# Kernel tuning notes

Hardware: AMD Instinct MI355X
Metric: run time of the kernel (lower is better)

## Reference

```python
import jax, jax.numpy as jnp
import numpy as np
from jax import lax

TOPK = 80
RADIUS_GAIN = 14.0
RADIUS_MIN = 1.5
RADIUS_MAX = 18.0


def _norm01(x, eps=1e-6):
    b = x.shape[0]
    flat = x.reshape(b, -1)
    mn = flat.min(axis=1).reshape(b, 1, 1, 1)
    mx = flat.max(axis=1).reshape(b, 1, 1, 1)
    return (x - mn) / (mx - mn + eps)


def _avg_pool9(x):
    # kernel 9, stride 1, pad 4, count_include_pad=True (torch default)
    s = lax.reduce_window(x, 0.0, lax.add, (1, 1, 9, 9), (1, 1, 1, 1),
                          [(0, 0), (0, 0), (4, 4), (4, 4)])
    return s / 81.0


def _max_pool5(x):
    return lax.reduce_window(x, -jnp.inf, lax.max, (1, 1, 5, 5), (1, 1, 1, 1),
                             [(0, 0), (0, 0), (2, 2), (2, 2)])


def setup_inputs() -> dict:
    key = jax.random.key(0)
    k1, k2 = jax.random.split(key)
    B, H, W = 8, 256, 256
    voxel_score_map = jax.random.uniform(k1, (B, 1, H, W), dtype=jnp.float32)
    depth = jax.random.uniform(k2, (B, 1, H, W), dtype=jnp.float32)
    return {"voxel_score_map": voxel_score_map, "depth": depth}


def reference(voxel_score_map, depth):
    dtype = voxel_score_map.dtype
    b, _, h, w = voxel_score_map.shape

    # _compact_connected_prior
    occ = (voxel_score_map > 0.2).astype(dtype)
    local_occ = _avg_pool9(occ)
    local_mass = _avg_pool9(voxel_score_map)
    compact = _norm01(local_occ * local_mass)
    score_map = voxel_score_map * compact

    # _gaussian_map: 5x5 max-pool NMS -> per-image top-k peaks
    pooled = _max_pool5(score_map)
    maxima = score_map * (score_map == pooled).astype(dtype)
    flat = maxima[:, 0].reshape(b, h * w)          # [b, h*w]
    vals, inds = lax.top_k(flat, TOPK)             # [b, k]
    vals = jnp.where(vals > 0, vals, jnp.zeros_like(vals))  # masked peaks splat 0
    ys = (inds // w).astype(dtype)
    xs = (inds % w).astype(dtype)

    z = jnp.take_along_axis(depth[:, 0].reshape(b, h * w), inds, axis=1)
    z = jnp.maximum(z, 0.001)
    radius = jnp.clip(RADIUS_GAIN / z, RADIUS_MIN, RADIUS_MAX)  # [b, k]
    sigma2 = (0.6 * radius) ** 2                                 # [b, k]

    yy = jnp.arange(h, dtype=dtype)
    xx = jnp.arange(w, dtype=dtype)
    dx = xx[None, None, None, :] - xs[:, :, None, None]   # [b, k, 1, w]
    dy = yy[None, None, :, None] - ys[:, :, None, None]   # [b, k, h, 1]
    d2 = dx ** 2 + dy ** 2                                 # [b, k, h, w]
    maps = vals[:, :, None, None] * jnp.exp(-d2 / (2.0 * sigma2[:, :, None, None] + 1e-6))
    gauss = maps.max(axis=1)[:, None]                      # [b, 1, h, w]
    return _norm01(gauss)
```

## Files before the change

kernel.cpp:

```cpp
#include <hip/hip_runtime.h>
#include <float.h>
#include <math.h>

#define BB 8
#define HH 256
#define WW 256
#define NPIX 65536
#define TOT (BB*NPIX)
#define KTOP 80
#define NTIL 64
#define TCAP 128
#define CAP 8192
#define SELBINS 4096
#define BNDCAP 4096
#define NBLK (BB*NTIL)
typedef unsigned long long ull;

__global__ void k_box9(const float* __restrict__ vsm, float* __restrict__ prod,
                       float* __restrict__ pmn, float* __restrict__ pmx,
                       unsigned* __restrict__ histg, unsigned* __restrict__ bcnt) {
    int blk = blockIdx.x;
    int b = blk >> 6, t = blk & 63;
    int ty0 = (t >> 3) << 5, tx0 = (t & 7) << 5;
    int tid = threadIdx.x;

    if (tid < 64) histg[b * SELBINS + t * 64 + tid] = 0u;
    if (blk < BB && tid == 0) bcnt[blk] = 0u;

    __shared__ float val[40][40];
    __shared__ float rs_o[40][32];
    __shared__ float rs_m[40][32];
    for (int i = tid; i < 1600; i += 256) {
        int ly = i / 40, lx = i - ly * 40;
        int gy = ty0 - 4 + ly, gx = tx0 - 4 + lx;
        float v = 0.f;
        if (gy >= 0 && gy < HH && gx >= 0 && gx < WW) v = vsm[(b * HH + gy) * WW + gx];
        val[ly][lx] = v;
    }
    __syncthreads();
    for (int i = tid; i < 1280; i += 256) {
        int ly = i >> 5, lx = i & 31;
        float so = 0.f, sm = 0.f;
        #pragma unroll
        for (int d = 0; d < 9; ++d) { float v = val[ly][lx + d]; so += (v > 0.2f) ? 1.f : 0.f; sm += v; }
        rs_o[ly][lx] = so; rs_m[ly][lx] = sm;
    }
    __syncthreads();
    int ox = tid & 31, oy0 = (tid >> 5) << 2;
    float tmn = FLT_MAX, tmx = -FLT_MAX;
    #pragma unroll
    for (int j = 0; j < 4; ++j) {
        int oy = oy0 + j;
        float so = 0.f, sm = 0.f;
        #pragma unroll
        for (int d = 0; d < 9; ++d) { so += rs_o[oy + d][ox]; sm += rs_m[oy + d][ox]; }
        float p = (so * (1.f / 81.f)) * (sm * (1.f / 81.f));
        prod[(b * HH + ty0 + oy) * WW + tx0 + ox] = p;
        tmn = fminf(tmn, p); tmx = fmaxf(tmx, p);
    }
    __shared__ float smn[256], smx[256];
    smn[tid] = tmn; smx[tid] = tmx;
    __syncthreads();
    for (int off = 128; off > 0; off >>= 1) {
        if (tid < off) { smn[tid] = fminf(smn[tid], smn[tid + off]); smx[tid] = fmaxf(smx[tid], smx[tid + off]); }
        __syncthreads();
    }
    if (tid == 0) { pmn[blk] = smn[0]; pmx[blk] = smx[0]; }
}

__global__ void k_nms(const float* __restrict__ vsm, const float* __restrict__ prod,
                      const float* __restrict__ pmn, const float* __restrict__ pmx,
                      unsigned* __restrict__ bcnt, float* __restrict__ candV,
                      int* __restrict__ candI, unsigned* __restrict__ histg) {
    int blk = blockIdx.x;
    int b = blk >> 6, t = blk & 63;
    int ty0 = (t >> 3) << 5, tx0 = (t & 7) << 5;
    int tid = threadIdx.x;
    __shared__ float sred[2];
    if (tid < 64) {
        float mn = pmn[b * NTIL + tid];
        float mx = pmx[b * NTIL + tid];
        #pragma unroll
        for (int o = 32; o > 0; o >>= 1) { mn = fminf(mn, __shfl_xor(mn, o, 64)); mx = fmaxf(mx, __shfl_xor(mx, o, 64)); }
        if (tid == 0) { sred[0] = mn; sred[1] = mx; }
    }
    __syncthreads();
    float mnp = sred[0];
    float inv = 1.f / (sred[1] - mnp + 1e-6f);
    __shared__ float sc[36][36];
    __shared__ float hm[36][32];
    for (int i = tid; i < 1296; i += 256) {
        int ly = i / 36, lx = i - ly * 36;
        int gy = ty0 - 2 + ly, gx = tx0 - 2 + lx;
        float s = -FLT_MAX;
        if (gy >= 0 && gy < HH && gx >= 0 && gx < WW) {
            int idx = (b * HH + gy) * WW + gx;
            s = vsm[idx] * ((prod[idx] - mnp) * inv);
        }
        sc[ly][lx] = s;
    }
    __syncthreads();
    for (int i = tid; i < 1152; i += 256) {
        int ly = i >> 5, lx = i & 31;
        float m = sc[ly][lx];
        #pragma unroll
        for (int d = 1; d < 5; ++d) m = fmaxf(m, sc[ly][lx + d]);
        hm[ly][lx] = m;
    }
    __syncthreads();
    __shared__ unsigned scnt;
    __shared__ unsigned sbase;
    __shared__ float bv[TCAP];
    __shared__ int bi[TCAP];
    if (tid == 0) scnt = 0;
    __syncthreads();
    int ox = tid & 31, oy0 = (tid >> 5) << 2;
    #pragma unroll
    for (int j = 0; j < 4; ++j) {
        int oy = oy0 + j;
        float m = hm[oy][ox];
        #pragma unroll
        for (int d = 1; d < 5; ++d) m = fmaxf(m, hm[oy + d][ox]);
        float s = sc[oy + 2][ox + 2];
        if (s == m && s > 0.f) {
            unsigned p = atomicAdd(&scnt, 1u);
            if (p < TCAP) { bv[p] = s; bi[p] = (ty0 + oy) * WW + tx0 + ox; }
        }
    }
    __syncthreads();
    unsigned cnt = min(scnt, (unsigned)TCAP);
    if (tid == 0) sbase = cnt ? atomicAdd(&bcnt[b], cnt) : 0u;
    __syncthreads();
    unsigned base = sbase;
    for (unsigned i = tid; i < cnt; i += 256) {
        unsigned pos = base + i;
        if (pos < CAP) {
            float v = bv[i];
            candV[b * CAP + pos] = v;
            candI[b * CAP + pos] = bi[i];
            atomicAdd(&histg[b * SELBINS + (__float_as_uint(v) >> 19)], 1u);
        }
    }
}

__global__ void __launch_bounds__(1024)
k_topk(const float* __restrict__ depth, const unsigned* __restrict__ bcnt,
       const float* __restrict__ candV, const int* __restrict__ candI,
       const unsigned* __restrict__ histg, float4* __restrict__ pk) {
    int b = blockIdx.x;
    int tid = threadIdx.x;
    __shared__ unsigned sc[1024];
    __shared__ ull bnd[BNDCAP];
    __shared__ ull acc[KTOP];
    __shared__ int sBin;
    __shared__ unsigned nAccS, nBndS;

    const unsigned* hg = histg + b * SELBINS;
    int j0 = tid * 4;
    unsigned h0 = hg[j0], h1 = hg[j0 + 1], h2 = hg[j0 + 2], h3 = hg[j0 + 3];
    unsigned part = h0 + h1 + h2 + h3;
    sc[tid] = part;
    if (tid == 0) { sBin = 0; nAccS = 0; nBndS = 0; }
    __syncthreads();
    for (int off = 1; off < 1024; off <<= 1) {
        unsigned v = (tid + off < 1024) ? sc[tid + off] : 0u;
        __syncthreads();
        sc[tid] += v;
        __syncthreads();
    }
    unsigned excl = sc[tid] - part;
    unsigned suf3 = excl + h3, suf2 = suf3 + h2, suf1 = suf2 + h1, suf0 = suf1 + h0;
    if (suf0 >= KTOP && suf0 - h0 < KTOP) sBin = j0;
    if (suf1 >= KTOP && suf1 - h1 < KTOP) sBin = j0 + 1;
    if (suf2 >= KTOP && suf2 - h2 < KTOP) sBin = j0 + 2;
    if (suf3 >= KTOP && suf3 - h3 < KTOP) sBin = j0 + 3;
    __syncthreads();
    int B = sBin;

    int nC = min((int)bcnt[b], CAP);
    for (int i = tid; i < nC; i += 1024) {
        float v = candV[b * CAP + i];
        unsigned bits = __float_as_uint(v);
        int bin = (int)(bits >> 19);
        if (bin >= B) {
            ull key = ((ull)bits << 32) | (ull)(0xFFFFFFFFu - (unsigned)candI[b * CAP + i]);
            if (bin > B) {
                unsigned p = atomicAdd(&nAccS, 1u);
                if (p < KTOP) acc[p] = key;
            } else {
                unsigned q = atomicAdd(&nBndS, 1u);
                if (q < BNDCAP) bnd[q] = key;
            }
        }
    }
    __syncthreads();
    unsigned nAcc = min(nAccS, (unsigned)KTOP);
    unsigned nBnd = min(nBndS, (unsigned)BNDCAP);
    unsigned quota = (KTOP > nAcc) ? (KTOP - nAcc) : 0u;
    if (quota > nBnd) quota = nBnd;

    for (int i = tid; i < (int)nBnd; i += 1024) {
        ull mykey = bnd[i];
        unsigned rank = 0;
        for (unsigned j = 0; j < nBnd; ++j) rank += (bnd[j] > mykey) ? 1u : 0u;
        if (rank < quota) acc[nAcc + rank] = mykey;
    }
    __syncthreads();

    if (tid < KTOP) {
        unsigned nTot = nAcc + quota;
        ull key = ((unsigned)tid < nTot) ? acc[tid] : 0ull;
        float plog = -INFINITY, fx = 0.f, fy = 0.f, c = 0.f;
        if (key) {
            unsigned bits = (unsigned)(key >> 32);
            int idx = (int)(0xFFFFFFFFu - (unsigned)(key & 0xFFFFFFFFu));
            float val = __uint_as_float(bits);
            plog = log2f(val);
            fx = (float)(idx & 255);
            fy = (float)(idx >> 8);
            float z = fmaxf(depth[b * NPIX + idx], 0.001f);
            float r = fminf(fmaxf(14.f / z, 1.5f), 18.f);
            float s2 = 0.36f * r * r;
            c = 1.44269504f / (2.f * s2 + 1e-6f);
        }
        pk[b * KTOP + tid] = make_float4(plog, fx, fy, c);
    }
}

__global__ void k_splat(const float4* __restrict__ pk, float* __restrict__ gauss,
                        float* __restrict__ gmn, float* __restrict__ gmx) {
    int blk = blockIdx.x;
    int b = blk >> 6;
    int y0 = (blk & 63) << 2;
    int x = threadIdx.x;
    __shared__ float4 lp[KTOP];
    if (x < KTOP) lp[x] = pk[b * KTOP + x];
    __syncthreads();
    float fx = (float)x, fy = (float)y0;
    float g0 = -INFINITY, g1 = -INFINITY, g2 = -INFINITY, g3 = -INFINITY;
    #pragma unroll 4
    for (int k = 0; k < KTOP; ++k) {
        float4 q = lp[k];
        float dx = fx - q.y;
        float dx2 = dx * dx;
        float dy = fy - q.z;
        float d2;
        d2 = fmaf(dy, dy, dx2);        g0 = fmaxf(g0, fmaf(-d2, q.w, q.x));
        float dyb = dy + 1.f;
        d2 = fmaf(dyb, dyb, dx2);      g1 = fmaxf(g1, fmaf(-d2, q.w, q.x));
        float dyc = dy + 2.f;
        d2 = fmaf(dyc, dyc, dx2);      g2 = fmaxf(g2, fmaf(-d2, q.w, q.x));
        float dyd = dy + 3.f;
        d2 = fmaf(dyd, dyd, dx2);      g3 = fmaxf(g3, fmaf(-d2, q.w, q.x));
    }
    float v0 = exp2f(g0), v1 = exp2f(g1), v2 = exp2f(g2), v3 = exp2f(g3);
    int base = (b * HH + y0) * WW + x;
    gauss[base] = v0; gauss[base + WW] = v1; gauss[base + 2 * WW] = v2; gauss[base + 3 * WW] = v3;
    float tmn = fminf(fminf(v0, v1), fminf(v2, v3));
    float tmx = fmaxf(fmaxf(v0, v1), fmaxf(v2, v3));
    __shared__ float smn[256], smx[256];
    smn[x] = tmn; smx[x] = tmx;
    __syncthreads();
    for (int off = 128; off > 0; off >>= 1) {
        if (x < off) { smn[x] = fminf(smn[x], smn[x + off]); smx[x] = fmaxf(smx[x], smx[x + off]); }
        __syncthreads();
    }
    if (x == 0) { gmn[blk] = smn[0]; gmx[blk] = smx[0]; }
}

__global__ void k_norm(const float* __restrict__ gauss, const float* __restrict__ gmn,
                       const float* __restrict__ gmx, float* __restrict__ out) {
    int blk = blockIdx.x;
    int b = blk >> 6;
    int tid = threadIdx.x;
    __shared__ float sred[2];
    if (tid < 64) {
        float mn = gmn[b * NTIL + tid];
        float mx = gmx[b * NTIL + tid];
        #pragma unroll
        for (int o = 32; o > 0; o >>= 1) { mn = fminf(mn, __shfl_xor(mn, o, 64)); mx = fmaxf(mx, __shfl_xor(mx, o, 64)); }
        if (tid == 0) { sred[0] = mn; sred[1] = mx; }
    }
    __syncthreads();
    float mn = sred[0];
    float inv = 1.f / (sred[1] - mn + 1e-6f);
    int i = blk * 256 + tid;
    float4 v = ((const float4*)gauss)[i];
    v.x = (v.x - mn) * inv;
    v.y = (v.y - mn) * inv;
    v.z = (v.z - mn) * inv;
    v.w = (v.w - mn) * inv;
    ((float4*)out)[i] = v;
}

extern "C" void kernel_launch(void* const* d_in, const int* in_sizes, int n_in,
                              void* d_out, int out_size, void* d_ws, size_t ws_size,
                              hipStream_t stream) {
    const float* vsm   = (const float*)d_in[0];
    const float* depth = (const float*)d_in[1];
    float* out = (float*)d_out;

    float4* pk   = (float4*)d_ws;
    float* prod  = (float*)(pk + BB * KTOP);
    float* gauss = prod + TOT;
    float* pmn   = gauss + TOT;
    float* pmx   = pmn + NBLK;
    float* gmn   = pmx + NBLK;
    float* gmx   = gmn + NBLK;
    unsigned* bcnt  = (unsigned*)(gmx + NBLK);
    unsigned* histg = bcnt + BB;
    float* candV = (float*)(histg + BB * SELBINS);
    int*   candI = (int*)(candV + BB * CAP);

    k_box9 <<<NBLK, 256, 0, stream>>>(vsm, prod, pmn, pmx, histg, bcnt);
    k_nms  <<<NBLK, 256, 0, stream>>>(vsm, prod, pmn, pmx, bcnt, candV, candI, histg);
    k_topk <<<BB, 1024, 0, stream>>>(depth, bcnt, candV, candI, histg, pk);
    k_splat<<<NBLK, 256, 0, stream>>>(pk, gauss, gmn, gmx);
    k_norm <<<NBLK, 256, 0, stream>>>(gauss, gmn, gmx, out);
}
```

Measured before the change: 42.96 us.

## Fold normalisation into splat using peak max and cull far peaks per row band

```diff
diff --git a/kernel.cpp b/kernel.cpp
--- a/kernel.cpp
+++ b/kernel.cpp
@@ -17,7 +17,7 @@
 typedef unsigned long long ull;
 
 __global__ void k_box9(const float* __restrict__ vsm, float* __restrict__ prod,
-                       float* __restrict__ pmn, float* __restrict__ pmx,
+                       float* __restrict__ pmn,
                        unsigned* __restrict__ histg, unsigned* __restrict__ bcnt) {
     int blk = blockIdx.x;
     int b = blk >> 6, t = blk & 63;
@@ -47,7 +47,7 @@
     }
     __syncthreads();
     int ox = tid & 31, oy0 = (tid >> 5) << 2;
-    float tmn = FLT_MAX, tmx = -FLT_MAX;
+    float tmn = FLT_MAX;
     #pragma unroll
     for (int j = 0; j < 4; ++j) {
         int oy = oy0 + j;
@@ -56,37 +56,33 @@
         for (int d = 0; d < 9; ++d) { so += rs_o[oy + d][ox]; sm += rs_m[oy + d][ox]; }
         float p = (so * (1.f / 81.f)) * (sm * (1.f / 81.f));
         prod[(b * HH + ty0 + oy) * WW + tx0 + ox] = p;
-        tmn = fminf(tmn, p); tmx = fmaxf(tmx, p);
-    }
-    __shared__ float smn[256], smx[256];
-    smn[tid] = tmn; smx[tid] = tmx;
-    __syncthreads();
-    for (int off = 128; off > 0; off >>= 1) {
-        if (tid < off) { smn[tid] = fminf(smn[tid], smn[tid + off]); smx[tid] = fmaxf(smx[tid], smx[tid + off]); }
-        __syncthreads();
-    }
-    if (tid == 0) { pmn[blk] = smn[0]; pmx[blk] = smx[0]; }
+        tmn = fminf(tmn, p);
+    }
+    #pragma unroll
+    for (int o = 32; o > 0; o >>= 1) tmn = fminf(tmn, __shfl_xor(tmn, o, 64));
+    __shared__ float wmn[4];
+    if ((tid & 63) == 0) wmn[tid >> 6] = tmn;
+    __syncthreads();
+    if (tid == 0) pmn[blk] = fminf(fminf(wmn[0], wmn[1]), fminf(wmn[2], wmn[3]));
 }
 
 __global__ void k_nms(const float* __restrict__ vsm, const float* __restrict__ prod,
-                      const float* __restrict__ pmn, const float* __restrict__ pmx,
+                      const float* __restrict__ pmn,
                       unsigned* __restrict__ bcnt, float* __restrict__ candV,
                       int* __restrict__ candI, unsigned* __restrict__ histg) {
     int blk = blockIdx.x;
     int b = blk >> 6, t = blk & 63;
     int ty0 = (t >> 3) << 5, tx0 = (t & 7) << 5;
     int tid = threadIdx.x;
-    __shared__ float sred[2];
+    __shared__ float sredn;
     if (tid < 64) {
         float mn = pmn[b * NTIL + tid];
-        float mx = pmx[b * NTIL + tid];
-        #pragma unroll
-        for (int o = 32; o > 0; o >>= 1) { mn = fminf(mn, __shfl_xor(mn, o, 64)); mx = fmaxf(mx, __shfl_xor(mx, o, 64)); }
-        if (tid == 0) { sred[0] = mn; sred[1] = mx; }
-    }
-    __syncthreads();
-    float mnp = sred[0];
-    float inv = 1.f / (sred[1] - mnp + 1e-6f);
+        #pragma unroll
+        for (int o = 32; o > 0; o >>= 1) mn = fminf(mn, __shfl_xor(mn, o, 64));
+        if (tid == 0) sredn = mn;
+    }
+    __syncthreads();
+    float mnp = sredn;
     __shared__ float sc[36][36];
     __shared__ float hm[36][32];
     for (int i = tid; i < 1296; i += 256) {
@@ -95,7 +91,7 @@
         float s = -FLT_MAX;
         if (gy >= 0 && gy < HH && gx >= 0 && gx < WW) {
             int idx = (b * HH + gy) * WW + gx;
-            s = vsm[idx] * ((prod[idx] - mnp) * inv);
+            s = vsm[idx] * (prod[idx] - mnp);
         }
         sc[ly][lx] = s;
     }
@@ -146,21 +142,22 @@
 __global__ void __launch_bounds__(1024)
 k_topk(const float* __restrict__ depth, const unsigned* __restrict__ bcnt,
        const float* __restrict__ candV, const int* __restrict__ candI,
-       const unsigned* __restrict__ histg, float4* __restrict__ pk) {
+       const unsigned* __restrict__ histg, float4* __restrict__ pk,
+       float* __restrict__ vmaxg) {
     int b = blockIdx.x;
     int tid = threadIdx.x;
     __shared__ unsigned sc[1024];
     __shared__ ull bnd[BNDCAP];
     __shared__ ull acc[KTOP];
     __shared__ int sBin;
-    __shared__ unsigned nAccS, nBndS;
+    __shared__ unsigned nAccS, nBndS, svm;
 
     const unsigned* hg = histg + b * SELBINS;
     int j0 = tid * 4;
     unsigned h0 = hg[j0], h1 = hg[j0 + 1], h2 = hg[j0 + 2], h3 = hg[j0 + 3];
     unsigned part = h0 + h1 + h2 + h3;
     sc[tid] = part;
-    if (tid == 0) { sBin = 0; nAccS = 0; nBndS = 0; }
+    if (tid == 0) { sBin = 0; nAccS = 0; nBndS = 0; svm = 0; }
     __syncthreads();
     for (int off = 1; off < 1024; off <<= 1) {
         unsigned v = (tid + off < 1024) ? sc[tid + off] : 0u;
@@ -207,12 +204,13 @@
     }
     __syncthreads();
 
+    unsigned nTot = nAcc + quota;
     if (tid < KTOP) {
-        unsigned nTot = nAcc + quota;
         ull key = ((unsigned)tid < nTot) ? acc[tid] : 0ull;
         float plog = -INFINITY, fx = 0.f, fy = 0.f, c = 0.f;
         if (key) {
             unsigned bits = (unsigned)(key >> 32);
+            atomicMax(&svm, bits);
             int idx = (int)(0xFFFFFFFFu - (unsigned)(key & 0xFFFFFFFFu));
             float val = __uint_as_float(bits);
             plog = log2f(val);
@@ -225,72 +223,63 @@
         }
         pk[b * KTOP + tid] = make_float4(plog, fx, fy, c);
     }
-}
-
-__global__ void k_splat(const float4* __restrict__ pk, float* __restrict__ gauss,
-                        float* __restrict__ gmn, float* __restrict__ gmx) {
+    __syncthreads();
+    if (tid == 0) vmaxg[b] = __uint_as_float(svm);
+}
+
+__global__ void __launch_bounds__(256)
+k_splat(const float4* __restrict__ pk, const float* __restrict__ vmaxg,
+        float* __restrict__ out) {
     int blk = blockIdx.x;
     int b = blk >> 6;
     int y0 = (blk & 63) << 2;
     int x = threadIdx.x;
     __shared__ float4 lp[KTOP];
+    __shared__ float4 lpf[KTOP];
+    __shared__ unsigned fcnt;
+    if (x == 0) fcnt = 0;
     if (x < KTOP) lp[x] = pk[b * KTOP + x];
     __syncthreads();
+
+    float vmax = vmaxg[b];
+    float thr = log2f(vmax + 1e-30f) - 11.f;
+
+    if (x < KTOP) {
+        float4 q = lp[x];
+        float dymin = 0.f;
+        if (q.z < (float)y0) dymin = (float)y0 - q.z;
+        else if (q.z > (float)(y0 + 3)) dymin = q.z - (float)(y0 + 3);
+        if (q.x - dymin * dymin * q.w >= thr) {
+            unsigned p = atomicAdd(&fcnt, 1u);
+            lpf[p] = q;
+        }
+    }
+    __syncthreads();
+    int m = (int)fcnt;
+
     float fx = (float)x, fy = (float)y0;
     float g0 = -INFINITY, g1 = -INFINITY, g2 = -INFINITY, g3 = -INFINITY;
     #pragma unroll 4
-    for (int k = 0; k < KTOP; ++k) {
-        float4 q = lp[k];
+    for (int k = 0; k < m; ++k) {
+        float4 q = lpf[k];
         float dx = fx - q.y;
         float dx2 = dx * dx;
         float dy = fy - q.z;
         float d2;
-        d2 = fmaf(dy, dy, dx2);        g0 = fmaxf(g0, fmaf(-d2, q.w, q.x));
+        d2 = fmaf(dy, dy, dx2);          g0 = fmaxf(g0, fmaf(-d2, q.w, q.x));
         float dyb = dy + 1.f;
-        d2 = fmaf(dyb, dyb, dx2);      g1 = fmaxf(g1, fmaf(-d2, q.w, q.x));
+        d2 = fmaf(dyb, dyb, dx2);        g1 = fmaxf(g1, fmaf(-d2, q.w, q.x));
         float dyc = dy + 2.f;
-        d2 = fmaf(dyc, dyc, dx2);      g2 = fmaxf(g2, fmaf(-d2, q.w, q.x));
+        d2 = fmaf(dyc, dyc, dx2);        g2 = fmaxf(g2, fmaf(-d2, q.w, q.x));
         float dyd = dy + 3.f;
-        d2 = fmaf(dyd, dyd, dx2);      g3 = fmaxf(g3, fmaf(-d2, q.w, q.x));
-    }
-    float v0 = exp2f(g0), v1 = exp2f(g1), v2 = exp2f(g2), v3 = exp2f(g3);
+        d2 = fmaf(dyd, dyd, dx2);        g3 = fmaxf(g3, fmaf(-d2, q.w, q.x));
+    }
+    float inv = 1.f / (vmax + 1e-6f);
     int base = (b * HH + y0) * WW + x;
-    gauss[base] = v0; gauss[base + WW] = v1; gauss[base + 2 * WW] = v2; gauss[base + 3 * WW] = v3;
-    float tmn = fminf(fminf(v0, v1), fminf(v2, v3));
-    float tmx = fmaxf(fmaxf(v0, v1), fmaxf(v2, v3));
-    __shared__ float smn[256], smx[256];
-    smn[x] = tmn; smx[x] = tmx;
-    __syncthreads();
-    for (int off = 128; off > 0; off >>= 1) {
-        if (x < off) { smn[x] = fminf(smn[x], smn[x + off]); smx[x] = fmaxf(smx[x], smx[x + off]); }
-        __syncthreads();
-    }
-    if (x == 0) { gmn[blk] = smn[0]; gmx[blk] = smx[0]; }
-}
-
-__global__ void k_norm(const float* __restrict__ gauss, const float* __restrict__ gmn,
-                       const float* __restrict__ gmx, float* __restrict__ out) {
-    int blk = blockIdx.x;
-    int b = blk >> 6;
-    int tid = threadIdx.x;
-    __shared__ float sred[2];
-    if (tid < 64) {
-        float mn = gmn[b * NTIL + tid];
-        float mx = gmx[b * NTIL + tid];
-        #pragma unroll
-        for (int o = 32; o > 0; o >>= 1) { mn = fminf(mn, __shfl_xor(mn, o, 64)); mx = fmaxf(mx, __shfl_xor(mx, o, 64)); }
-        if (tid == 0) { sred[0] = mn; sred[1] = mx; }
-    }
-    __syncthreads();
-    float mn = sred[0];
-    float inv = 1.f / (sred[1] - mn + 1e-6f);
-    int i = blk * 256 + tid;
-    float4 v = ((const float4*)gauss)[i];
-    v.x = (v.x - mn) * inv;
-    v.y = (v.y - mn) * inv;
-    v.z = (v.z - mn) * inv;
-    v.w = (v.w - mn) * inv;
-    ((float4*)out)[i] = v;
+    out[base]          = exp2f(g0) * inv;
+    out[base + WW]     = exp2f(g1) * inv;
+    out[base + 2 * WW] = exp2f(g2) * inv;
+    out[base + 3 * WW] = exp2f(g3) * inv;
 }
 
 extern "C" void kernel_launch(void* const* d_in, const int* in_sizes, int n_in,
@@ -301,20 +290,16 @@
     float* out = (float*)d_out;
 
     float4* pk   = (float4*)d_ws;
-    float* prod  = (float*)(pk + BB * KTOP);
-    float* gauss = prod + TOT;
-    float* pmn   = gauss + TOT;
-    float* pmx   = pmn + NBLK;
-    float* gmn   = pmx + NBLK;
-    float* gmx   = gmn + NBLK;
-    unsigned* bcnt  = (unsigned*)(gmx + NBLK);
+    float* vmaxg = (float*)(pk + BB * KTOP);
+    float* prod  = vmaxg + BB;
+    float* pmn   = prod + TOT;
+    unsigned* bcnt  = (unsigned*)(pmn + NBLK);
     unsigned* histg = bcnt + BB;
     float* candV = (float*)(histg + BB * SELBINS);
     int*   candI = (int*)(candV + BB * CAP);
 
-    k_box9 <<<NBLK, 256, 0, stream>>>(vsm, prod, pmn, pmx, histg, bcnt);
-    k_nms  <<<NBLK, 256, 0, stream>>>(vsm, prod, pmn, pmx, bcnt, candV, candI, histg);
-    k_topk <<<BB, 1024, 0, stream>>>(depth, bcnt, candV, candI, histg, pk);
-    k_splat<<<NBLK, 256, 0, stream>>>(pk, gauss, gmn, gmx);
-    k_norm <<<NBLK, 256, 0, stream>>>(gauss, gmn, gmx, out);
-}
+    k_box9 <<<NBLK, 256, 0, stream>>>(vsm, prod, pmn, histg, bcnt);
+    k_nms  <<<NBLK, 256, 0, stream>>>(vsm, prod, pmn, bcnt, candV, candI, histg);
+    k_topk <<<BB, 1024, 0, stream>>>(depth, bcnt, candV, candI, histg, pk, vmaxg);
+    k_splat<<<NBLK, 256, 0, stream>>>(pk, vmaxg, out);
+}
```

After: 38.80 us. -9.7%, faster.
